# Kernel optimization log

Measured on AMD Instinct MI355X. Metric: run time of the kernel, lower is better.

## Reference

```python
import jax, jax.numpy as jnp
import numpy as np
from jax import lax

RIVER_LENGTH = 50000.0
NUM_SEGMENTS = 20
DT = 3600.0
DX = RIVER_LENGTH / NUM_SEGMENTS
CFL = min(2.0 * DT / DX, 0.9)  # c=2.0 hard-coded in original; clipped to 0.9


def setup_inputs() -> dict:
    key = jax.random.key(0)
    ks = jax.random.split(key, 5)
    B, T = 8192, 4096
    return {
        "runoff": jax.random.uniform(ks[0], (B, T), dtype=jnp.float32) * 10.0,  # mm/hr
        "basin_area": jax.random.uniform(ks[1], (B, 1), dtype=jnp.float32) * 1000.0 + 10.0,  # km^2
        "manning_n": jax.random.uniform(ks[2], (B, 1), dtype=jnp.float32) * 0.05 + 0.01,
        "slope": jax.random.uniform(ks[3], (B, 1), dtype=jnp.float32) * 0.01 + 1e-4,
        "width": jax.random.uniform(ks[4], (B, 1), dtype=jnp.float32) * 50.0 + 1.0,
    }


def reference(runoff, basin_area, manning_n, slope, width):
    # lateral inflow per segment: mm/hr -> m^3/s over basin area, split into segments
    area_m2 = basin_area * 1e6  # (B,1)
    q_lateral = runoff / 1000.0 / 3600.0 * area_m2 / float(NUM_SEGMENTS)  # (B,T)

    B = runoff.shape[0]
    Q0 = jnp.zeros((B, NUM_SEGMENTS + 1), dtype=runoff.dtype)

    def step(Q, q_in):
        # upwind update for segments 1..N using OLD state (matches tf version)
        q_in = q_in[:, None]  # (B,1)
        Q_upd = jnp.maximum(Q[:, 1:] - CFL * (Q[:, 1:] - Q[:, :-1]) + q_in * DT, 0.0)
        Q_new = jnp.concatenate([Q[:, :1], Q_upd], axis=1)  # segment 0 unchanged (stays 0)
        return Q_new, Q_new[:, -1]

    _, outlet = lax.scan(step, Q0, q_lateral.T)  # outlet: (T,B)
    return outlet.T  # (B,T) discharge in m^3/s
```

## Files before the change

### kernel.cpp

```cpp
#include <hip/hip_runtime.h>


#define KTAPS 32
#define RPT   8
#define TPB   256
#define TILE_T (TPB * RPT)
#define NQ   ((TILE_T + KTAPS) / 4)

struct WTab { float w[KTAPS]; };

__device__ __forceinline__ int swz(int q) { return q ^ ((q >> 3) & 7); }

__global__ __launch_bounds__(TPB) void kwr_fir_lds_kernel(
    const float* __restrict__ runoff,
    const float* __restrict__ basin_area,
    float* __restrict__ out,
    int T, int tiles_per_row, WTab wt)
{
    __shared__ float4 lds[NQ];

    const int tid  = threadIdx.x;
    const int blk  = blockIdx.x;
    const int b    = blk / tiles_per_row;
    const int tile = blk - b * tiles_per_row;
    const long long rowbase = (long long)b * T;
    const int tstart = tile * TILE_T - KTAPS;

    const float4* gsrc = (const float4*)(runoff + rowbase + tstart);
    #pragma unroll
    for (int pass = 0; pass < 3; ++pass) {
        int q = tid + pass * TPB;
        if (q < NQ) {
            float4 v;
            if (tstart + 4 * q >= 0) v = gsrc[q];
            else                     v = make_float4(0.f, 0.f, 0.f, 0.f);
            lds[swz(q)] = v;
        }
    }
    __syncthreads();

    float buf[RPT + KTAPS];
    #pragma unroll
    for (int c = 0; c < (RPT + KTAPS) / 4; ++c) {
        float4 v = lds[swz(2 * tid + c)];
        buf[4*c+0] = v.x; buf[4*c+1] = v.y;
        buf[4*c+2] = v.z; buf[4*c+3] = v.w;
    }

    float acc[RPT];
    #pragma unroll
    for (int r = 0; r < RPT; ++r) acc[r] = 0.0f;

    #pragma unroll
    for (int k = 0; k < KTAPS; ++k) {
        const float wk = wt.w[k];
        #pragma unroll
        for (int r = 0; r < RPT; ++r)
            acc[r] = fmaf(wk, buf[KTAPS + r - k], acc[r]);
    }

    const float s = basin_area[b] * 50.0f;
    float* orow = out + rowbase + tile * TILE_T + tid * RPT;
    ((float4*)orow)[0] = make_float4(acc[0]*s, acc[1]*s, acc[2]*s, acc[3]*s);
    ((float4*)orow)[1] = make_float4(acc[4]*s, acc[5]*s, acc[6]*s, acc[7]*s);
}

extern "C" void kernel_launch(void* const* d_in, const int* in_sizes, int n_in,
                              void* d_out, int out_size, void* d_ws, size_t ws_size,
                              hipStream_t stream)
{
    const float* runoff     = (const float*)d_in[0];
    const float* basin_area = (const float*)d_in[1];
    float* out = (float*)d_out;

    const int B = in_sizes[1];
    const int T = in_sizes[0] / B;

    WTab wt;
    double Q[21];
    for (int j = 0; j <= 20; ++j) Q[j] = (j >= 1) ? 1.0 : 0.0;
    wt.w[0] = 1.0f;
    for (int k = 1; k < KTAPS; ++k) {
        for (int j = 20; j >= 1; --j) Q[j] = 0.1 * Q[j] + 0.9 * Q[j - 1];
        wt.w[k] = (float)Q[20];
    }

    const int tiles_per_row = T / TILE_T;
    const int nblk = B * tiles_per_row;

    kwr_fir_lds_kernel<<<nblk, TPB, 0, stream>>>(runoff, basin_area, out,
                                                 T, tiles_per_row, wt);
}
```

Before: 233.9 us.

## Replace 32-tap FIR with sliding-window sum plus short weighted tail

The FIR weights for taps 1..19 equal exactly 1.0 (the step response saturates once the wave has crossed the segments), so the sum over those taps becomes a running sliding-window sum. Only a small tail of non-unit weights, taps 20..25, is still applied with FMAs. Outputs per thread rise from 8 to 16, which halves the block count and amortizes the halo. Taps beyond 25 are dropped, and the running sum may accumulate fp32 rounding differently from the direct sum.

```diff
diff --git a/kernel.cpp b/kernel.cpp
--- a/kernel.cpp
+++ b/kernel.cpp
@@ -1,68 +1,72 @@
 #include <hip/hip_runtime.h>
 
 
-#define KTAPS 32
-#define RPT   8
-#define TPB   256
+#define KTAIL  6
+#define HALO   32
+#define RPT    16
+#define TPB    256
 #define TILE_T (TPB * RPT)
-#define NQ   ((TILE_T + KTAPS) / 4)
+#define NQ     ((TILE_T + HALO) / 4)
 
-struct WTab { float w[KTAPS]; };
+struct WTail { float w[KTAIL]; };
 
 __device__ __forceinline__ int swz(int q) { return q ^ ((q >> 3) & 7); }
 
-__global__ __launch_bounds__(TPB) void kwr_fir_lds_kernel(
+__global__ __launch_bounds__(TPB) void kwr_slide_kernel(
     const float* __restrict__ runoff,
     const float* __restrict__ basin_area,
     float* __restrict__ out,
-    int T, int tiles_per_row, WTab wt)
+    int T, int tiles_per_row, WTail wt)
 {
     __shared__ float4 lds[NQ];
 
     const int tid  = threadIdx.x;
-    const int blk  = blockIdx.x;
-    const int b    = blk / tiles_per_row;
-    const int tile = blk - b * tiles_per_row;
+    const int b    = blockIdx.x / tiles_per_row;
+    const int tile = blockIdx.x - b * tiles_per_row;
     const long long rowbase = (long long)b * T;
-    const int tstart = tile * TILE_T - KTAPS;
+    const int tstart = tile * TILE_T - HALO;
 
     const float4* gsrc = (const float4*)(runoff + rowbase + tstart);
     #pragma unroll
-    for (int pass = 0; pass < 3; ++pass) {
+    for (int pass = 0; pass < (NQ + TPB - 1) / TPB; ++pass) {
         int q = tid + pass * TPB;
         if (q < NQ) {
-            float4 v;
-            if (tstart + 4 * q >= 0) v = gsrc[q];
-            else                     v = make_float4(0.f, 0.f, 0.f, 0.f);
+            float4 v = (tstart + 4 * q >= 0) ? gsrc[q]
+                                             : make_float4(0.f, 0.f, 0.f, 0.f);
             lds[swz(q)] = v;
         }
     }
     __syncthreads();
 
-    float buf[RPT + KTAPS];
+    float buf[RPT + HALO];
     #pragma unroll
-    for (int c = 0; c < (RPT + KTAPS) / 4; ++c) {
-        float4 v = lds[swz(2 * tid + c)];
+    for (int c = 0; c < (RPT + HALO) / 4; ++c) {
+        float4 v = lds[swz(4 * tid + c)];
         buf[4*c+0] = v.x; buf[4*c+1] = v.y;
         buf[4*c+2] = v.z; buf[4*c+3] = v.w;
     }
 
-    float acc[RPT];
+    float S = 0.0f;
     #pragma unroll
-    for (int r = 0; r < RPT; ++r) acc[r] = 0.0f;
+    for (int i = 13; i <= 32; ++i) S += buf[i];
 
+    float res[RPT];
     #pragma unroll
-    for (int k = 0; k < KTAPS; ++k) {
-        const float wk = wt.w[k];
+    for (int r = 0; r < RPT; ++r) {
+        if (r > 0) S += buf[32 + r] - buf[12 + r];
+        float v = S;
         #pragma unroll
-        for (int r = 0; r < RPT; ++r)
-            acc[r] = fmaf(wk, buf[KTAPS + r - k], acc[r]);
+        for (int k = 0; k < KTAIL; ++k)
+            v = fmaf(wt.w[k], buf[12 + r - k], v);
+        res[r] = v;
     }
 
     const float s = basin_area[b] * 50.0f;
     float* orow = out + rowbase + tile * TILE_T + tid * RPT;
-    ((float4*)orow)[0] = make_float4(acc[0]*s, acc[1]*s, acc[2]*s, acc[3]*s);
-    ((float4*)orow)[1] = make_float4(acc[4]*s, acc[5]*s, acc[6]*s, acc[7]*s);
+    #pragma unroll
+    for (int g = 0; g < RPT / 4; ++g)
+        ((float4*)orow)[g] = make_float4(res[4*g+0]*s, res[4*g+1]*s,
+                                         res[4*g+2]*s, res[4*g+3]*s);
 }
 
 extern "C" void kernel_launch(void* const* d_in, const int* in_sizes, int n_in,
@@ -76,18 +80,17 @@
     const int B = in_sizes[1];
     const int T = in_sizes[0] / B;
 
-    WTab wt;
+    WTail wt;
     double Q[21];
     for (int j = 0; j <= 20; ++j) Q[j] = (j >= 1) ? 1.0 : 0.0;
-    wt.w[0] = 1.0f;
-    for (int k = 1; k < KTAPS; ++k) {
+    for (int k = 1; k <= 25; ++k) {
         for (int j = 20; j >= 1; --j) Q[j] = 0.1 * Q[j] + 0.9 * Q[j - 1];
-        wt.w[k] = (float)Q[20];
+        if (k >= 20) wt.w[k - 20] = (float)Q[20];
     }
 
     const int tiles_per_row = T / TILE_T;
     const int nblk = B * tiles_per_row;
 
-    kwr_fir_lds_kernel<<<nblk, TPB, 0, stream>>>(runoff, basin_area, out,
-                                                 T, tiles_per_row, wt);
+    kwr_slide_kernel<<<nblk, TPB, 0, stream>>>(runoff, basin_area, out,
+                                               T, tiles_per_row, wt);
 }
```

After: 254.2 us. 1.09x slower.
